# Optimization experiments

Hardware: AMD Instinct MI355X
Metric: run time of the kernel (lower is better)

## Reference

```python
import jax, jax.numpy as jnp
import numpy as np

NUM_HEADS = 8
MASK_RATE = 0.5


def setup_inputs() -> dict:
    key = jax.random.key(0)
    ks = jax.random.split(key, 6)
    B, N, C = 8, 1024, 256
    TABLE = 10
    att_embedding = jax.random.normal(ks[0], (B, N, C), dtype=jnp.float32)
    relation_position = jax.random.randint(ks[1], (B, N, N), 0, TABLE, dtype=jnp.int32)
    rel_len = jax.random.randint(ks[2], (B,), 0, 20, dtype=jnp.int32)
    W_qkv = jax.random.normal(ks[3], (C, 3 * C), dtype=jnp.float32) * (1.0 / np.sqrt(C))
    W_proj = jax.random.normal(ks[4], (C, C), dtype=jnp.float32) * (1.0 / np.sqrt(C))
    b_proj = jnp.zeros((C,), dtype=jnp.float32)
    bias_table = jax.random.normal(ks[5], (TABLE, NUM_HEADS), dtype=jnp.float32) * 0.02
    return {
        "att_embedding": att_embedding,
        "relation_position": relation_position,
        "rel_len": rel_len,
        "W_qkv": W_qkv,
        "W_proj": W_proj,
        "b_proj": b_proj,
        "bias_table": bias_table,
    }


def reference(att_embedding, relation_position, rel_len, W_qkv, W_proj, b_proj, bias_table):
    B, N, C = att_embedding.shape
    H = NUM_HEADS
    hd = C // H
    scale = hd ** -0.5

    # QKV projection (no bias): [B,N,3C] -> q,k,v each [B,H,N,hd]
    qkv = (att_embedding @ W_qkv).reshape(B, N, 3, H, hd)
    qkv = jnp.transpose(qkv, (2, 0, 3, 1, 4))
    q, k, v = qkv[0], qkv[1], qkv[2]

    # Attention scores [B,H,N,N]
    attn = jnp.einsum("bhnd,bhmd->bhnm", q, k) * scale

    # Relative position bias: gather [B,N,N,H] -> [B,H,N,N]
    pos_bias = jnp.transpose(bias_table[relation_position], (0, 3, 1, 2))

    # Mask bias: table row t gets -100 iff t > mask_len (mask_len+1 .. TABLE-1);
    # identical across heads -> compute as [B,1,N,N] instead of materializing [B,H,N,N].
    mask_len = (rel_len.astype(jnp.float32) * MASK_RATE).astype(jnp.int32)
    mask_bias = jnp.where(relation_position > mask_len[:, None, None], -100.0, 0.0)[:, None]

    attn = jax.nn.softmax(attn + pos_bias + mask_bias, axis=-1)

    # Weighted values -> [B,N,C] -> output projection
    x = jnp.einsum("bhnm,bhmd->bnhd", attn, v).reshape(B, N, C)
    x = x @ W_proj + b_proj
    return x
```

## Files before the change

kernel.cpp:

```cpp
#include <hip/hip_runtime.h>
#include <hip/hip_bf16.h>

typedef __bf16 bf16;
typedef __bf16 bf16x2 __attribute__((ext_vector_type(2)));
typedef __bf16 bf16x8 __attribute__((ext_vector_type(8)));
typedef float f32x4 __attribute__((ext_vector_type(4)));
typedef int i32x4 __attribute__((ext_vector_type(4)));

#define B_ 8
#define N_ 1024
#define C_ 256
#define H_ 8
#define C3_ 768
#define SCALE 0.17677669529663689f
#define FMAX 16.0f


__global__ __launch_bounds__(256) void prep(
    const float* __restrict__ Wqkv, const float* __restrict__ Wproj,
    bf16* __restrict__ Wq_tiled, bf16* __restrict__ Wp_tiled)
{
  int bb = blockIdx.x;
  int o = bb * 256 + threadIdx.x;
  if (bb < 768) {
    int kk = o & 31;
    int idx = o >> 5;
    int nr = idx & 63;
    int qq = idx >> 6;
    int nt = qq % 12, kt = qq / 12;
    int n = nt * 64 + nr, k = kt * 32 + kk;
    Wq_tiled[o] = (bf16)Wqkv[k * C3_ + n];
  } else {
    int p = o - 768 * 256;
    int kk = p & 31;
    int n = (p >> 5) & 255;
    int kt = p >> 13;
    int k = kt * 32 + kk;
    Wp_tiled[p] = (bf16)Wproj[k * C_ + n];
  }
}

__global__ __launch_bounds__(256) void gemm_qkv(
    const float* __restrict__ A, const bf16* __restrict__ Wq_tiled,
    bf16* __restrict__ q, bf16* __restrict__ kT, bf16* __restrict__ vT)
{
  __shared__ bf16 As[128][40];
  __shared__ bf16 Bts[128][40];
  __shared__ bf16 Vls[64][136];

  int tid = threadIdx.x;
  int wave = tid >> 6, lane = tid & 63, quad = lane >> 4, l16 = lane & 15;
  int m0 = blockIdx.x * 128, n0 = blockIdx.y * 128;
  int msub = (wave & 1) * 64, nsub = (wave >> 1) * 64;

  f32x4 acc[4][4] = {};

  int arow = tid >> 1, akc = (tid & 1) * 16;
  const float* aptr = A + (long)(m0 + arow) * C_ + akc;
  int bn = tid >> 1, bkc = (tid & 1) * 16;
  const bf16* bptr = Wq_tiled +
      ((long)(blockIdx.y * 2 + (bn >> 6)) * 2048 + (bn & 63) * 32 + bkc);

  float4 a0 = *reinterpret_cast<const float4*>(aptr);
  float4 a1 = *reinterpret_cast<const float4*>(aptr + 4);
  float4 a2 = *reinterpret_cast<const float4*>(aptr + 8);
  float4 a3 = *reinterpret_cast<const float4*>(aptr + 12);
  i32x4 bv0 = *reinterpret_cast<const i32x4*>(bptr);
  i32x4 bv1 = *reinterpret_cast<const i32x4*>(bptr + 8);

  for (int kt = 0; kt < 8; ++kt) {
    __syncthreads();
    {
      bf16 at[16] = {(bf16)a0.x, (bf16)a0.y, (bf16)a0.z, (bf16)a0.w,
                     (bf16)a1.x, (bf16)a1.y, (bf16)a1.z, (bf16)a1.w,
                     (bf16)a2.x, (bf16)a2.y, (bf16)a2.z, (bf16)a2.w,
                     (bf16)a3.x, (bf16)a3.y, (bf16)a3.z, (bf16)a3.w};
      *reinterpret_cast<bf16x8*>(&As[arow][akc]) = *reinterpret_cast<bf16x8*>(at);
      *reinterpret_cast<bf16x8*>(&As[arow][akc + 8]) = *reinterpret_cast<bf16x8*>(at + 8);
      *reinterpret_cast<i32x4*>(&Bts[bn][bkc]) = bv0;
      *reinterpret_cast<i32x4*>(&Bts[bn][bkc + 8]) = bv1;
    }
    __syncthreads();

    if (kt < 7) {
      int kn = (kt + 1) * 32;
      a0 = *reinterpret_cast<const float4*>(aptr + kn);
      a1 = *reinterpret_cast<const float4*>(aptr + kn + 4);
      a2 = *reinterpret_cast<const float4*>(aptr + kn + 8);
      a3 = *reinterpret_cast<const float4*>(aptr + kn + 12);
      bv0 = *reinterpret_cast<const i32x4*>(bptr + (long)(kt + 1) * 24576);
      bv1 = *reinterpret_cast<const i32x4*>(bptr + (long)(kt + 1) * 24576 + 8);
    }

    bf16x8 af[4], bfr[4];
#pragma unroll
    for (int mi = 0; mi < 4; ++mi)
      af[mi] = *reinterpret_cast<const bf16x8*>(&As[msub + mi * 16 + l16][quad * 8]);
#pragma unroll
    for (int ni = 0; ni < 4; ++ni)
      bfr[ni] = *reinterpret_cast<const bf16x8*>(&Bts[nsub + ni * 16 + l16][quad * 8]);
#pragma unroll
    for (int mi = 0; mi < 4; ++mi)
#pragma unroll
      for (int ni = 0; ni < 4; ++ni)
        acc[mi][ni] = __builtin_amdgcn_mfma_f32_16x16x32_bf16(af[mi], bfr[ni], acc[mi][ni], 0, 0, 0);
  }

  if (n0 < 256) {
#pragma unroll
    for (int mi = 0; mi < 4; ++mi)
#pragma unroll
      for (int ni = 0; ni < 4; ++ni)
#pragma unroll
        for (int r = 0; r < 4; ++r) {
          int row = m0 + msub + mi * 16 + quad * 4 + r;
          int col = n0 + nsub + ni * 16 + l16;
          q[(long)row * 256 + col] = (bf16)(acc[mi][ni][r] * SCALE);
        }
  } else if (n0 < 512) {
#pragma unroll
    for (int mi = 0; mi < 4; ++mi)
#pragma unroll
      for (int ni = 0; ni < 4; ++ni)
#pragma unroll
        for (int r = 0; r < 4; ++r) {
          int row = m0 + msub + mi * 16 + quad * 4 + r;
          int c = n0 + nsub + ni * 16 + l16 - 256;
          int b = row >> 10, n = row & 1023;
          int h = c >> 5, d = c & 31;
          kT[(((long)(b * H_ + h)) * N_ + n) * 32 + d] = (bf16)acc[mi][ni][r];
        }
  } else {
    int b = m0 >> 10;
#pragma unroll
    for (int ch = 0; ch < 2; ++ch) {
      __syncthreads();
      if ((nsub >> 6) == ch) {
#pragma unroll
        for (int mi = 0; mi < 4; ++mi)
#pragma unroll
          for (int ni = 0; ni < 4; ++ni)
#pragma unroll
            for (int r = 0; r < 4; ++r) {
              int cc = ni * 16 + l16;
              int nn = msub + mi * 16 + quad * 4 + r;
              int np = (nn & 96) | (2 * (nn & 15)) | ((nn >> 4) & 1);
              Vls[cc][np] = (bf16)acc[mi][ni][r];
            }
      }
      __syncthreads();
      int cc = tid >> 2, nseg = (tid & 3) * 32;
      long base = ((long)(b * C_ + (n0 - 512) + ch * 64 + cc)) * N_ + (m0 & 1023) + nseg;
#pragma unroll
      for (int j = 0; j < 4; ++j)
        *reinterpret_cast<i32x4*>(vT + base + j * 8) =
            *reinterpret_cast<const i32x4*>(&Vls[cc][nseg + j * 8]);
    }
  }
}

__global__ __launch_bounds__(512) void flash_attn(
    const bf16* __restrict__ q, const bf16* __restrict__ kT,
    const bf16* __restrict__ vT, const int* __restrict__ rel,
    const int* __restrict__ rel_len, const float* __restrict__ btab,
    const bf16* __restrict__ Wp_tiled, const float* __restrict__ bias,
    float* __restrict__ out)
{
  __shared__ bf16 Vs[256][40];
  __shared__ unsigned RelsP[4][33];
  __shared__ bf16 Pls[H_][16 * 40];
  __shared__ float btl[H_][16];
  __shared__ bf16 attL[16][264];

  int tid = threadIdx.x;
  int h = tid >> 6, lane = tid & 63, quad = lane >> 4, l16 = lane & 15;
  int b = blockIdx.y, i0 = blockIdx.x * 16;
  long bN = (long)b * N_;

  int mask_len = (int)((float)rel_len[b] * 0.5f);
  if (tid < 80) {
    int t = tid >> 3, hh = tid & 7;
    btl[hh][t] = btab[t * H_ + hh] + (t > mask_len ? -100.f : 0.f) - FMAX;
  }

  bf16x8 qf = *reinterpret_cast<const bf16x8*>(
      q + (bN + i0 + l16) * 256 + h * 32 + quad * 8);

  const bf16* kbase = kT + ((long)(b * H_ + h)) * N_ * 32 + quad * 8;
  int vrow = tid >> 1, voff = (tid & 1) * 16;
  const bf16* vgp = vT + ((long)b * C_ + vrow) * N_ + voff;
  int rg = (tid >> 5) & 3, rcol = tid & 31;
  const int* rgp = rel + (bN + i0 + rg * 4) * N_ + rcol;

  bf16x8 kf0 = *reinterpret_cast<const bf16x8*>(kbase + (long)l16 * 32);
  bf16x8 kf1 = *reinterpret_cast<const bf16x8*>(kbase + (long)(16 + l16) * 32);
  bf16x8 vr0 = *reinterpret_cast<const bf16x8*>(vgp);
  bf16x8 vr1 = *reinterpret_cast<const bf16x8*>(vgp + 8);
  int rr0 = 0, rr1 = 0, rr2 = 0, rr3 = 0;
  if (tid < 128) {
    rr0 = rgp[0]; rr1 = rgp[N_]; rr2 = rgp[2 * N_]; rr3 = rgp[3 * N_];
  }

  f32x4 oacc[2] = {};
  float l_part[4] = {0.f, 0.f, 0.f, 0.f};

  for (int j0 = 0; j0 < N_; j0 += 32) {
    __syncthreads();
    *reinterpret_cast<bf16x8*>(&Vs[vrow][voff]) = vr0;
    *reinterpret_cast<bf16x8*>(&Vs[vrow][voff + 8]) = vr1;
    if (tid < 128)
      RelsP[rg][rcol] = (unsigned)rr0 | ((unsigned)rr1 << 8) |
                        ((unsigned)rr2 << 16) | ((unsigned)rr3 << 24);
    __syncthreads();

    int jn = j0 + 32; jn = (jn < N_) ? jn : 0;
    bf16x8 kn0 = *reinterpret_cast<const bf16x8*>(kbase + (long)(jn + l16) * 32);
    bf16x8 kn1 = *reinterpret_cast<const bf16x8*>(kbase + (long)(jn + 16 + l16) * 32);
    vr0 = *reinterpret_cast<const bf16x8*>(vgp + jn);
    vr1 = *reinterpret_cast<const bf16x8*>(vgp + jn + 8);
    if (tid < 128) {
      rr0 = rgp[jn]; rr1 = rgp[N_ + jn];
      rr2 = rgp[2 * N_ + jn]; rr3 = rgp[3 * N_ + jn];
    }

    f32x4 z = {};
    f32x4 s0 = __builtin_amdgcn_mfma_f32_16x16x32_bf16(qf, kf0, z, 0, 0, 0);
    f32x4 s1 = __builtin_amdgcn_mfma_f32_16x16x32_bf16(qf, kf1, z, 0, 0, 0);
    kf0 = kn0; kf1 = kn1;

    unsigned w0 = RelsP[quad][l16];
    unsigned w1 = RelsP[quad][16 + l16];
#pragma unroll
    for (int r = 0; r < 4; ++r) {
      int il = quad * 4 + r;
      int rv0 = (w0 >> (8 * r)) & 255;
      int rv1 = (w1 >> (8 * r)) & 255;
      float p0 = __expf(s0[r] + btl[h][rv0]);
      float p1 = __expf(s1[r] + btl[h][rv1]);
      l_part[r] += p0 + p1;
      bf16x2 pp = {(bf16)p0, (bf16)p1};
      *reinterpret_cast<bf16x2*>(&Pls[h][il * 40 + l16 * 2]) = pp;
    }
    asm volatile("s_waitcnt lgkmcnt(0)" ::: "memory");
    bf16x8 pf = *reinterpret_cast<const bf16x8*>(&Pls[h][l16 * 40 + quad * 8]);
    bf16x8 vf0 = *reinterpret_cast<const bf16x8*>(&Vs[h * 32 + l16][quad * 8]);
    bf16x8 vf1 = *reinterpret_cast<const bf16x8*>(&Vs[h * 32 + 16 + l16][quad * 8]);
    oacc[0] = __builtin_amdgcn_mfma_f32_16x16x32_bf16(pf, vf0, oacc[0], 0, 0, 0);
    oacc[1] = __builtin_amdgcn_mfma_f32_16x16x32_bf16(pf, vf1, oacc[1], 0, 0, 0);
  }

#pragma unroll
  for (int r = 0; r < 4; ++r) {
    float l = l_part[r];
#pragma unroll
    for (int m = 1; m < 16; m <<= 1) l += __shfl_xor(l, m);
    float inv = 1.f / l;
    attL[quad * 4 + r][h * 32 + l16] = (bf16)(oacc[0][r] * inv);
    attL[quad * 4 + r][h * 32 + 16 + l16] = (bf16)(oacc[1][r] * inv);
  }
  __syncthreads();

  f32x4 pacc[2] = {};
  const bf16* wp = Wp_tiled + ((h * 32 + l16) * 32 + quad * 8);
#pragma unroll
  for (int kt = 0; kt < 8; ++kt) {
    bf16x8 afr = *reinterpret_cast<const bf16x8*>(&attL[l16][kt * 32 + quad * 8]);
    bf16x8 b0 = *reinterpret_cast<const bf16x8*>(wp + kt * 8192);
    bf16x8 b1 = *reinterpret_cast<const bf16x8*>(wp + kt * 8192 + 512);
    pacc[0] = __builtin_amdgcn_mfma_f32_16x16x32_bf16(afr, b0, pacc[0], 0, 0, 0);
    pacc[1] = __builtin_amdgcn_mfma_f32_16x16x32_bf16(afr, b1, pacc[1], 0, 0, 0);
  }
  float bi0 = bias[h * 32 + l16];
  float bi1 = bias[h * 32 + 16 + l16];
#pragma unroll
  for (int r = 0; r < 4; ++r) {
    long rowoff = (bN + i0 + quad * 4 + r) * C_ + h * 32;
    out[rowoff + l16] = pacc[0][r] + bi0;
    out[rowoff + 16 + l16] = pacc[1][r] + bi1;
  }
}

extern "C" void kernel_launch(void* const* d_in, const int* in_sizes, int n_in,
                              void* d_out, int out_size, void* d_ws, size_t ws_size,
                              hipStream_t stream) {
  const float* X     = (const float*)d_in[0];
  const int*   rel   = (const int*)d_in[1];
  const int*   rlen  = (const int*)d_in[2];
  const float* Wqkv  = (const float*)d_in[3];
  const float* Wproj = (const float*)d_in[4];
  const float* bproj = (const float*)d_in[5];
  const float* btab  = (const float*)d_in[6];
  float* out = (float*)d_out;

  char* ws = (char*)d_ws;
  bf16* Wq_tiled = (bf16*)ws;
  bf16* Wp_tiled = (bf16*)(ws + 393216);
  bf16* q  = (bf16*)(ws + 524288);
  bf16* kT = (bf16*)(ws + 524288 + 4194304);
  bf16* vT = (bf16*)(ws + 524288 + 2 * 4194304);

  prep<<<dim3(1024), 256, 0, stream>>>(Wqkv, Wproj, Wq_tiled, Wp_tiled);
  gemm_qkv<<<dim3(8192 / 128, C3_ / 128), 256, 0, stream>>>(X, Wq_tiled, q, kT, vT);
  flash_attn<<<dim3(N_ / 16, B_), 512, 0, stream>>>(
      q, kT, vT, rel, rlen, btab, Wp_tiled, bproj, out);
}
```

Measured before the change: 144.3 us.

## Drop shared-memory staging in attention loop; load K/V/rel directly into registers with deeper prefetch

The attention main loop no longer stages V and the relation indices through shared memory with two block-wide barriers per 32-key step. Each wave now loads its own V fragments and rel indices straight from global memory into registers, double-buffering K/V and prefetching rel four tiles ahead. A workgroup-index swizzle remaps blocks across batches, and launch bounds request 4 blocks per CU. The aim is to remove the per-iteration barriers and LDS traffic, at the cost of higher register pressure and more redundant global loads of rel (int32 per element instead of packed bytes).

```diff
diff --git a/kernel.cpp b/kernel.cpp
--- a/kernel.cpp
+++ b/kernel.cpp
@@ -159,22 +159,23 @@
   }
 }
 
-__global__ __launch_bounds__(512) void flash_attn(
+__global__ __launch_bounds__(512, 4) void flash_attn(
     const bf16* __restrict__ q, const bf16* __restrict__ kT,
     const bf16* __restrict__ vT, const int* __restrict__ rel,
     const int* __restrict__ rel_len, const float* __restrict__ btab,
     const bf16* __restrict__ Wp_tiled, const float* __restrict__ bias,
     float* __restrict__ out)
 {
-  __shared__ bf16 Vs[256][40];
-  __shared__ unsigned RelsP[4][33];
   __shared__ bf16 Pls[H_][16 * 40];
   __shared__ float btl[H_][16];
   __shared__ bf16 attL[16][264];
 
   int tid = threadIdx.x;
   int h = tid >> 6, lane = tid & 63, quad = lane >> 4, l16 = lane & 15;
-  int b = blockIdx.y, i0 = blockIdx.x * 16;
+
+  int wg = blockIdx.y * 64 + blockIdx.x;
+  int swz = (wg & 7) * 64 + (wg >> 3);
+  int b = swz >> 6, i0 = (swz & 63) * 16;
   long bN = (long)b * N_;
 
   int mask_len = (int)((float)rel_len[b] * 0.5f);
@@ -182,71 +183,66 @@
     int t = tid >> 3, hh = tid & 7;
     btl[hh][t] = btab[t * H_ + hh] + (t > mask_len ? -100.f : 0.f) - FMAX;
   }
+  __syncthreads();
 
   bf16x8 qf = *reinterpret_cast<const bf16x8*>(
       q + (bN + i0 + l16) * 256 + h * 32 + quad * 8);
 
-  const bf16* kbase = kT + ((long)(b * H_ + h)) * N_ * 32 + quad * 8;
-  int vrow = tid >> 1, voff = (tid & 1) * 16;
-  const bf16* vgp = vT + ((long)b * C_ + vrow) * N_ + voff;
-  int rg = (tid >> 5) & 3, rcol = tid & 31;
-  const int* rgp = rel + (bN + i0 + rg * 4) * N_ + rcol;
-
-  bf16x8 kf0 = *reinterpret_cast<const bf16x8*>(kbase + (long)l16 * 32);
-  bf16x8 kf1 = *reinterpret_cast<const bf16x8*>(kbase + (long)(16 + l16) * 32);
-  bf16x8 vr0 = *reinterpret_cast<const bf16x8*>(vgp);
-  bf16x8 vr1 = *reinterpret_cast<const bf16x8*>(vgp + 8);
-  int rr0 = 0, rr1 = 0, rr2 = 0, rr3 = 0;
-  if (tid < 128) {
-    rr0 = rgp[0]; rr1 = rgp[N_]; rr2 = rgp[2 * N_]; rr3 = rgp[3 * N_];
-  }
+  const bf16* kb_ = kT + ((long)(b * H_ + h)) * N_ * 32 + quad * 8;
+  const bf16* vb_ = vT + ((long)b * C_ + h * 32 + l16) * N_ + quad * 8;
+  const int*  rb_ = rel + (bN + i0 + quad * 4) * N_ + l16;
+
+#define W_(J) ((J) < N_ ? (J) : 0)
+
+#define LDK(K0, K1, V0, V1, J) do {                                          \
+    K0 = *reinterpret_cast<const bf16x8*>(kb_ + (long)((J) + l16) * 32);     \
+    K1 = *reinterpret_cast<const bf16x8*>(kb_ + (long)((J) + 16 + l16) * 32);\
+    V0 = *reinterpret_cast<const bf16x8*>(vb_ + (J));                        \
+    V1 = *reinterpret_cast<const bf16x8*>(vb_ + 16 * N_ + (J));              \
+  } while (0)
+
+#define LDR(RV, J) do {                                                      \
+    _Pragma("unroll")                                                        \
+    for (int r = 0; r < 4; ++r) {                                            \
+      RV[2 * r]     = rb_[r * N_ + (J)];                                     \
+      RV[2 * r + 1] = rb_[r * N_ + (J) + 16];                                \
+    }                                                                        \
+  } while (0)
+
+#define COMP(K0, K1, V0, V1, RV) do {                                        \
+    f32x4 z = {};                                                            \
+    f32x4 s0 = __builtin_amdgcn_mfma_f32_16x16x32_bf16(qf, K0, z, 0, 0, 0);  \
+    f32x4 s1 = __builtin_amdgcn_mfma_f32_16x16x32_bf16(qf, K1, z, 0, 0, 0);  \
+    _Pragma("unroll")                                                        \
+    for (int r = 0; r < 4; ++r) {                                            \
+      float p0 = __expf(s0[r] + btl[h][RV[2 * r]]);                          \
+      float p1 = __expf(s1[r] + btl[h][RV[2 * r + 1]]);                      \
+      l_part[r] += p0 + p1;                                                  \
+      bf16x2 pp = {(bf16)p0, (bf16)p1};    \
+      *reinterpret_cast<bf16x2*>(&Pls[h][(quad * 4 + r) * 40 + l16 * 2]) = pp;\
+    }                                                                        \
+    asm volatile("s_waitcnt lgkmcnt(0)" ::: "memory");                       \
+    bf16x8 pf = *reinterpret_cast<const bf16x8*>(&Pls[h][l16 * 40 + quad * 8]);\
+    oacc[0] = __builtin_amdgcn_mfma_f32_16x16x32_bf16(pf, V0, oacc[0], 0, 0, 0);\
+    oacc[1] = __builtin_amdgcn_mfma_f32_16x16x32_bf16(pf, V1, oacc[1], 0, 0, 0);\
+  } while (0)
 
   f32x4 oacc[2] = {};
   float l_part[4] = {0.f, 0.f, 0.f, 0.f};
 
-  for (int j0 = 0; j0 < N_; j0 += 32) {
-    __syncthreads();
-    *reinterpret_cast<bf16x8*>(&Vs[vrow][voff]) = vr0;
-    *reinterpret_cast<bf16x8*>(&Vs[vrow][voff + 8]) = vr1;
-    if (tid < 128)
-      RelsP[rg][rcol] = (unsigned)rr0 | ((unsigned)rr1 << 8) |
-                        ((unsigned)rr2 << 16) | ((unsigned)rr3 << 24);
-    __syncthreads();
-
-    int jn = j0 + 32; jn = (jn < N_) ? jn : 0;
-    bf16x8 kn0 = *reinterpret_cast<const bf16x8*>(kbase + (long)(jn + l16) * 32);
-    bf16x8 kn1 = *reinterpret_cast<const bf16x8*>(kbase + (long)(jn + 16 + l16) * 32);
-    vr0 = *reinterpret_cast<const bf16x8*>(vgp + jn);
-    vr1 = *reinterpret_cast<const bf16x8*>(vgp + jn + 8);
-    if (tid < 128) {
-      rr0 = rgp[jn]; rr1 = rgp[N_ + jn];
-      rr2 = rgp[2 * N_ + jn]; rr3 = rgp[3 * N_ + jn];
-    }
-
-    f32x4 z = {};
-    f32x4 s0 = __builtin_amdgcn_mfma_f32_16x16x32_bf16(qf, kf0, z, 0, 0, 0);
-    f32x4 s1 = __builtin_amdgcn_mfma_f32_16x16x32_bf16(qf, kf1, z, 0, 0, 0);
-    kf0 = kn0; kf1 = kn1;
-
-    unsigned w0 = RelsP[quad][l16];
-    unsigned w1 = RelsP[quad][16 + l16];
-#pragma unroll
-    for (int r = 0; r < 4; ++r) {
-      int il = quad * 4 + r;
-      int rv0 = (w0 >> (8 * r)) & 255;
-      int rv1 = (w1 >> (8 * r)) & 255;
-      float p0 = __expf(s0[r] + btl[h][rv0]);
-      float p1 = __expf(s1[r] + btl[h][rv1]);
-      l_part[r] += p0 + p1;
-      bf16x2 pp = {(bf16)p0, (bf16)p1};
-      *reinterpret_cast<bf16x2*>(&Pls[h][il * 40 + l16 * 2]) = pp;
-    }
-    asm volatile("s_waitcnt lgkmcnt(0)" ::: "memory");
-    bf16x8 pf = *reinterpret_cast<const bf16x8*>(&Pls[h][l16 * 40 + quad * 8]);
-    bf16x8 vf0 = *reinterpret_cast<const bf16x8*>(&Vs[h * 32 + l16][quad * 8]);
-    bf16x8 vf1 = *reinterpret_cast<const bf16x8*>(&Vs[h * 32 + 16 + l16][quad * 8]);
-    oacc[0] = __builtin_amdgcn_mfma_f32_16x16x32_bf16(pf, vf0, oacc[0], 0, 0, 0);
-    oacc[1] = __builtin_amdgcn_mfma_f32_16x16x32_bf16(pf, vf1, oacc[1], 0, 0, 0);
+  bf16x8 ka0, ka1, vA0, vA1, kb0, kb1, vB0, vB1;
+  int r0[8], r1[8], r2[8], r3[8];
+
+  LDK(ka0, ka1, vA0, vA1, 0);
+  LDK(kb0, kb1, vB0, vB1, 32);
+  LDR(r0, 0); LDR(r1, 32); LDR(r2, 64); LDR(r3, 96);
+
+#pragma unroll 1
+  for (int j0 = 0; j0 < N_; j0 += 128) {
+    COMP(ka0, ka1, vA0, vA1, r0); LDK(ka0, ka1, vA0, vA1, W_(j0 + 64));  LDR(r0, W_(j0 + 128));
+    COMP(kb0, kb1, vB0, vB1, r1); LDK(kb0, kb1, vB0, vB1, W_(j0 + 96));  LDR(r1, W_(j0 + 160));
+    COMP(ka0, ka1, vA0, vA1, r2); LDK(ka0, ka1, vA0, vA1, W_(j0 + 128)); LDR(r2, W_(j0 + 192));
+    COMP(kb0, kb1, vB0, vB1, r3); LDK(kb0, kb1, vB0, vB1, W_(j0 + 160)); LDR(r3, W_(j0 + 224));
   }
 
 #pragma unroll
@@ -278,6 +274,10 @@
     out[rowoff + l16] = pacc[0][r] + bi0;
     out[rowoff + 16 + l16] = pacc[1][r] + bi1;
   }
+#undef W_
+#undef LDK
+#undef LDR
+#undef COMP
 }
 
 extern "C" void kernel_launch(void* const* d_in, const int* in_sizes, int n_in,
```

New measurement: 184.0 us. +27.5%, slower.

## Double-buffer V and rel tiles in flash attention, one barrier per step

Applied to the files above, without the earlier changes.

Replaces the single shared V/rel-position buffers with ping-pong buffers, so each iteration writes the next tile while reading the current one. This drops from two __syncthreads to one s_barrier per 32-column step, and global prefetch now runs two tiles ahead. It also remaps workgroup IDs so consecutive blocks are spread across batches. The cost is extra LDS use, which may lower occupancy, and more registers live across the loop.

```diff
diff --git a/kernel.cpp b/kernel.cpp
--- a/kernel.cpp
+++ b/kernel.cpp
@@ -166,15 +166,18 @@
     const bf16* __restrict__ Wp_tiled, const float* __restrict__ bias,
     float* __restrict__ out)
 {
-  __shared__ bf16 Vs[256][40];
-  __shared__ unsigned RelsP[4][33];
+  __shared__ bf16 Vs[2][256][40];
+  __shared__ unsigned RelsP[2][4][33];
   __shared__ bf16 Pls[H_][16 * 40];
   __shared__ float btl[H_][16];
   __shared__ bf16 attL[16][264];
 
   int tid = threadIdx.x;
   int h = tid >> 6, lane = tid & 63, quad = lane >> 4, l16 = lane & 15;
-  int b = blockIdx.y, i0 = blockIdx.x * 16;
+
+  int wg = blockIdx.y * 64 + blockIdx.x;
+  int swz = (wg & 7) * 64 + (wg >> 3);
+  int b = swz >> 6, i0 = (swz & 63) * 16;
   long bN = (long)b * N_;
 
   int mask_len = (int)((float)rel_len[b] * 0.5f);
@@ -192,62 +195,84 @@
   int rg = (tid >> 5) & 3, rcol = tid & 31;
   const int* rgp = rel + (bN + i0 + rg * 4) * N_ + rcol;
 
-  bf16x8 kf0 = *reinterpret_cast<const bf16x8*>(kbase + (long)l16 * 32);
-  bf16x8 kf1 = *reinterpret_cast<const bf16x8*>(kbase + (long)(16 + l16) * 32);
+  f32x4 oacc[2] = {};
+  float l_part[4] = {0.f, 0.f, 0.f, 0.f};
+
   bf16x8 vr0 = *reinterpret_cast<const bf16x8*>(vgp);
   bf16x8 vr1 = *reinterpret_cast<const bf16x8*>(vgp + 8);
   int rr0 = 0, rr1 = 0, rr2 = 0, rr3 = 0;
   if (tid < 128) {
     rr0 = rgp[0]; rr1 = rgp[N_]; rr2 = rgp[2 * N_]; rr3 = rgp[3 * N_];
   }
-
-  f32x4 oacc[2] = {};
-  float l_part[4] = {0.f, 0.f, 0.f, 0.f};
-
-  for (int j0 = 0; j0 < N_; j0 += 32) {
-    __syncthreads();
-    *reinterpret_cast<bf16x8*>(&Vs[vrow][voff]) = vr0;
-    *reinterpret_cast<bf16x8*>(&Vs[vrow][voff + 8]) = vr1;
-    if (tid < 128)
-      RelsP[rg][rcol] = (unsigned)rr0 | ((unsigned)rr1 << 8) |
-                        ((unsigned)rr2 << 16) | ((unsigned)rr3 << 24);
-    __syncthreads();
-
-    int jn = j0 + 32; jn = (jn < N_) ? jn : 0;
-    bf16x8 kn0 = *reinterpret_cast<const bf16x8*>(kbase + (long)(jn + l16) * 32);
-    bf16x8 kn1 = *reinterpret_cast<const bf16x8*>(kbase + (long)(jn + 16 + l16) * 32);
-    vr0 = *reinterpret_cast<const bf16x8*>(vgp + jn);
-    vr1 = *reinterpret_cast<const bf16x8*>(vgp + jn + 8);
-    if (tid < 128) {
-      rr0 = rgp[jn]; rr1 = rgp[N_ + jn];
-      rr2 = rgp[2 * N_ + jn]; rr3 = rgp[3 * N_ + jn];
-    }
-
-    f32x4 z = {};
-    f32x4 s0 = __builtin_amdgcn_mfma_f32_16x16x32_bf16(qf, kf0, z, 0, 0, 0);
-    f32x4 s1 = __builtin_amdgcn_mfma_f32_16x16x32_bf16(qf, kf1, z, 0, 0, 0);
-    kf0 = kn0; kf1 = kn1;
-
-    unsigned w0 = RelsP[quad][l16];
-    unsigned w1 = RelsP[quad][16 + l16];
-#pragma unroll
-    for (int r = 0; r < 4; ++r) {
-      int il = quad * 4 + r;
-      int rv0 = (w0 >> (8 * r)) & 255;
-      int rv1 = (w1 >> (8 * r)) & 255;
-      float p0 = __expf(s0[r] + btl[h][rv0]);
-      float p1 = __expf(s1[r] + btl[h][rv1]);
-      l_part[r] += p0 + p1;
-      bf16x2 pp = {(bf16)p0, (bf16)p1};
-      *reinterpret_cast<bf16x2*>(&Pls[h][il * 40 + l16 * 2]) = pp;
-    }
-    asm volatile("s_waitcnt lgkmcnt(0)" ::: "memory");
-    bf16x8 pf = *reinterpret_cast<const bf16x8*>(&Pls[h][l16 * 40 + quad * 8]);
-    bf16x8 vf0 = *reinterpret_cast<const bf16x8*>(&Vs[h * 32 + l16][quad * 8]);
-    bf16x8 vf1 = *reinterpret_cast<const bf16x8*>(&Vs[h * 32 + 16 + l16][quad * 8]);
-    oacc[0] = __builtin_amdgcn_mfma_f32_16x16x32_bf16(pf, vf0, oacc[0], 0, 0, 0);
-    oacc[1] = __builtin_amdgcn_mfma_f32_16x16x32_bf16(pf, vf1, oacc[1], 0, 0, 0);
-  }
+  *reinterpret_cast<bf16x8*>(&Vs[0][vrow][voff]) = vr0;
+  *reinterpret_cast<bf16x8*>(&Vs[0][vrow][voff + 8]) = vr1;
+  if (tid < 128)
+    RelsP[0][rg][rcol] = (unsigned)rr0 | ((unsigned)rr1 << 8) |
+                         ((unsigned)rr2 << 16) | ((unsigned)rr3 << 24);
+  vr0 = *reinterpret_cast<const bf16x8*>(vgp + 32);
+  vr1 = *reinterpret_cast<const bf16x8*>(vgp + 40);
+  if (tid < 128) {
+    rr0 = rgp[32]; rr1 = rgp[N_ + 32]; rr2 = rgp[2 * N_ + 32]; rr3 = rgp[3 * N_ + 32];
+  }
+  bf16x8 kf0 = *reinterpret_cast<const bf16x8*>(kbase + (long)l16 * 32);
+  bf16x8 kf1 = *reinterpret_cast<const bf16x8*>(kbase + (long)(16 + l16) * 32);
+  asm volatile("s_waitcnt lgkmcnt(0)" ::: "memory");
+  __builtin_amdgcn_s_barrier();
+
+#define W_(J) ((J) < N_ ? (J) : 0)
+
+#define FA_BODY(CUR, NXT, J0) do {                                            \
+    *reinterpret_cast<bf16x8*>(&Vs[NXT][vrow][voff]) = vr0;                   \
+    *reinterpret_cast<bf16x8*>(&Vs[NXT][vrow][voff + 8]) = vr1;               \
+    if (tid < 128)                                                            \
+      RelsP[NXT][rg][rcol] = (unsigned)rr0 | ((unsigned)rr1 << 8) |           \
+                             ((unsigned)rr2 << 16) | ((unsigned)rr3 << 24);   \
+    {                                                                         \
+      int j2 = W_((J0) + 64);                                                 \
+      vr0 = *reinterpret_cast<const bf16x8*>(vgp + j2);                       \
+      vr1 = *reinterpret_cast<const bf16x8*>(vgp + j2 + 8);                   \
+      if (tid < 128) {                                                        \
+        rr0 = rgp[j2]; rr1 = rgp[N_ + j2];                                    \
+        rr2 = rgp[2 * N_ + j2]; rr3 = rgp[3 * N_ + j2];                       \
+      }                                                                       \
+    }                                                                         \
+    int jn = W_((J0) + 32);                                                   \
+    bf16x8 kn0 = *reinterpret_cast<const bf16x8*>(kbase + (long)(jn + l16) * 32);      \
+    bf16x8 kn1 = *reinterpret_cast<const bf16x8*>(kbase + (long)(jn + 16 + l16) * 32); \
+    f32x4 z = {};                                                             \
+    f32x4 s0 = __builtin_amdgcn_mfma_f32_16x16x32_bf16(qf, kf0, z, 0, 0, 0);  \
+    f32x4 s1 = __builtin_amdgcn_mfma_f32_16x16x32_bf16(qf, kf1, z, 0, 0, 0);  \
+    kf0 = kn0; kf1 = kn1;                                                     \
+    unsigned w0 = RelsP[CUR][quad][l16];                                      \
+    unsigned w1 = RelsP[CUR][quad][16 + l16];                                 \
+    _Pragma("unroll")                                                         \
+    for (int r = 0; r < 4; ++r) {                                             \
+      int il = quad * 4 + r;                                                  \
+      int rv0 = (w0 >> (8 * r)) & 255;                                        \
+      int rv1 = (w1 >> (8 * r)) & 255;                                        \
+      float p0 = __expf(s0[r] + btl[h][rv0]);                                 \
+      float p1 = __expf(s1[r] + btl[h][rv1]);                                 \
+      l_part[r] += p0 + p1;                                                   \
+      bf16x2 pp = {(bf16)p0, (bf16)p1};     \
+      *reinterpret_cast<bf16x2*>(&Pls[h][il * 40 + l16 * 2]) = pp;            \
+    }                                                                         \
+    asm volatile("s_waitcnt lgkmcnt(0)" ::: "memory");                        \
+    bf16x8 pf = *reinterpret_cast<const bf16x8*>(&Pls[h][l16 * 40 + quad * 8]);        \
+    bf16x8 vf0 = *reinterpret_cast<const bf16x8*>(&Vs[CUR][h * 32 + l16][quad * 8]);   \
+    bf16x8 vf1 = *reinterpret_cast<const bf16x8*>(&Vs[CUR][h * 32 + 16 + l16][quad * 8]); \
+    oacc[0] = __builtin_amdgcn_mfma_f32_16x16x32_bf16(pf, vf0, oacc[0], 0, 0, 0);      \
+    oacc[1] = __builtin_amdgcn_mfma_f32_16x16x32_bf16(pf, vf1, oacc[1], 0, 0, 0);      \
+    asm volatile("s_waitcnt lgkmcnt(0)" ::: "memory");                        \
+    __builtin_amdgcn_s_barrier();                                             \
+  } while (0)
+
+#pragma unroll 1
+  for (int j0 = 0; j0 < N_; j0 += 64) {
+    FA_BODY(0, 1, j0);
+    FA_BODY(1, 0, j0 + 32);
+  }
+#undef FA_BODY
+#undef W_
 
 #pragma unroll
   for (int r = 0; r < 4; ++r) {
```

Measured after the change: 141.7 us. Within noise of the previous version (-1.7%).
